# Performance work log

Hardware: AMD Instinct MI355X
Metric: run time of the kernel (lower is better)

The kernel has to match this reference:

```python
import jax, jax.numpy as jnp
import numpy as np

N_HEAD = 8
D_HEAD = 64
HIDDEN = 512
T = 2048
BS = 4
SCALE = D_HEAD ** -0.5


def setup_inputs() -> dict:
    key = jax.random.key(0)
    k1, k2, k3 = jax.random.split(key, 3)
    x = jax.random.normal(k1, (BS, T, HIDDEN), dtype=jnp.float32)
    # torch Linear weight is (out,in); we store as (in,out) for x @ W
    W_qkv = jax.random.normal(k2, (HIDDEN, (2 * N_HEAD + 1) * D_HEAD), dtype=jnp.float32) * 0.02
    W_out = jax.random.normal(k3, (D_HEAD, HIDDEN), dtype=jnp.float32) * 0.02
    return {"x": x, "W_qkv": W_qkv, "W_out": W_out}


def reference(x, W_qkv, W_out):
    bs, t, h = x.shape
    qkv = x @ W_qkv  # (bs, t, (2H+1)*d)
    q, k, v = jnp.split(qkv, [N_HEAD * D_HEAD, 2 * N_HEAD * D_HEAD], axis=-1)
    q = q.reshape(bs, t, N_HEAD, D_HEAD)
    k = k.reshape(bs, t, N_HEAD, D_HEAD)
    # v is shared across heads: (bs, t, d)
    score = jnp.einsum("bqhd,bkhd->bhqk", q, k) * SCALE
    causal = jnp.triu(jnp.full((t, t), -jnp.inf, dtype=score.dtype), 1)
    score = score + causal[None, None, :, :]
    prob = jax.nn.softmax(score, axis=-1)  # (bs, H, t, t)
    attn_vec = jnp.einsum("bhqk,bkd->bhqd", prob, v)  # shared V broadcast over heads
    m_attn_vec = jnp.mean(attn_vec, axis=1)  # head-mean: (bs, t, d)
    out = m_attn_vec @ W_out  # (bs, t, hidden)
    return out, attn_vec
```

## Files before the change

### kernel.cpp

```cpp
#include <hip/hip_runtime.h>
#include <hip/hip_bf16.h>

#define NHEAD  8
#define DHEAD  64
#define HIDDEN 512
#define SEQ_T  2048
#define BATCH  4
#define NQKV   1088
#define QPITCH 1152
#define NT     32
#define NROWS  (BATCH * SEQ_T)
#define NBH    (BATCH * NHEAD)
#define LPITCH (NBH * SEQ_T)
#define OSLICE ((size_t)NBH * SEQ_T * DHEAD)
#define QSC    (0.125f * 1.44269504f)

typedef __attribute__((ext_vector_type(8))) short short8;
typedef __attribute__((ext_vector_type(4))) float f32x4;

__device__ __forceinline__ unsigned short f2bf(float f) {
  unsigned int u = __float_as_uint(f);
  u += 0x7FFFu + ((u >> 16) & 1u);
  return (unsigned short)(u >> 16);
}
__device__ __forceinline__ float bf2f(unsigned short u) {
  return __uint_as_float((unsigned int)u << 16);
}

__device__ __forceinline__ void load_lds16(const unsigned short* g, unsigned short* l) {
  __builtin_amdgcn_global_load_lds((const __attribute__((address_space(1))) void*)g,
                                   (__attribute__((address_space(3))) void*)l, 16, 0, 0);
}

__global__ __launch_bounds__(256) void prep(const float* __restrict__ x,
                                            const float* __restrict__ W,
                                            const float* __restrict__ Wout,
                                            unsigned short* __restrict__ xb,
                                            unsigned short* __restrict__ Wt,
                                            unsigned short* __restrict__ Wob) {
  const int bx = blockIdx.x;
  const int tid = threadIdx.x;
  if (bx < 2048) {
    const size_t i0 = ((size_t)bx * 256 + tid) * 8;
    float4 a = *(const float4*)(x + i0);
    float4 b = *(const float4*)(x + i0 + 4);
    ushort4 u0, u1;
    u0.x = f2bf(a.x); u0.y = f2bf(a.y); u0.z = f2bf(a.z); u0.w = f2bf(a.w);
    u1.x = f2bf(b.x); u1.y = f2bf(b.y); u1.z = f2bf(b.z); u1.w = f2bf(b.w);
    *(ushort4*)(xb + i0) = u0;
    *(ushort4*)(xb + i0 + 4) = u1;
    return;
  }
  if (bx >= 2184 && bx < 2192) {
    const int z = bx - 2184;
    const size_t base = (size_t)NQKV * HIDDEN + ((size_t)z * 256 + tid) * 16;
    uint4 zero = {0u, 0u, 0u, 0u};
    *(uint4*)(Wt + base) = zero;
    *(uint4*)(Wt + base + 8) = zero;
    return;
  }
  if (bx >= 2192) {
    const int n0 = (bx - 2192) * 64;
    __shared__ float T[64 * 65];
#pragma unroll
    for (int i = 0; i < 4; ++i) {
      int f = tid + i * 256;
      int r = f >> 4;
      int c4 = (f & 15) * 4;
      float4 v = *(const float4*)(Wout + (size_t)r * HIDDEN + n0 + c4);
      T[r * 65 + c4 + 0] = v.x;
      T[r * 65 + c4 + 1] = v.y;
      T[r * 65 + c4 + 2] = v.z;
      T[r * 65 + c4 + 3] = v.w;
    }
    __syncthreads();
#pragma unroll
    for (int i = 0; i < 4; ++i) {
      int f = tid + i * 256;
      int n = f >> 4;
      int k4 = (f & 15) * 4;
      ushort4 u;
      u.x = f2bf(T[(k4 + 0) * 65 + n]);
      u.y = f2bf(T[(k4 + 1) * 65 + n]);
      u.z = f2bf(T[(k4 + 2) * 65 + n]);
      u.w = f2bf(T[(k4 + 3) * 65 + n]);
      *(ushort4*)(Wob + (size_t)(n0 + n) * DHEAD + k4) = u;
    }
    return;
  }
  const int idx = bx - 2048;
  const int n0 = (idx % 17) * 64;
  const int k0 = (idx / 17) * 64;
  __shared__ float T[64 * 65];
#pragma unroll
  for (int i = 0; i < 4; ++i) {
    int f = tid + i * 256;
    int r = f >> 4;
    int c4 = (f & 15) * 4;
    float4 v = *(const float4*)(W + (size_t)(k0 + r) * NQKV + n0 + c4);
    T[r * 65 + c4 + 0] = v.x;
    T[r * 65 + c4 + 1] = v.y;
    T[r * 65 + c4 + 2] = v.z;
    T[r * 65 + c4 + 3] = v.w;
  }
  __syncthreads();
#pragma unroll
  for (int i = 0; i < 4; ++i) {
    int f = tid + i * 256;
    int n = f >> 4;
    int k4 = (f & 15) * 4;
    ushort4 u;
    u.x = f2bf(T[(k4 + 0) * 65 + n]);
    u.y = f2bf(T[(k4 + 1) * 65 + n]);
    u.z = f2bf(T[(k4 + 2) * 65 + n]);
    u.w = f2bf(T[(k4 + 3) * 65 + n]);
    *(ushort4*)(Wt + (size_t)(n0 + n) * HIDDEN + k0 + k4) = u;
  }
}

__global__ __launch_bounds__(256, 3) void qkv_mfma(const unsigned short* __restrict__ Xb,
                                                   const unsigned short* __restrict__ Wt,
                                                   unsigned short* __restrict__ Y,
                                                   unsigned short* __restrict__ vt) {
  __shared__ __align__(16) unsigned short SH[2 * 128 * 64];
  unsigned short* As = SH;
  unsigned short* Bs = SH + 128 * 64;
  const int L = blockIdx.x;
  const int slot = L >> 3;
  const int bm = (L & 7) * 8 + (slot & 7);
  const int bn = slot >> 3;
  const int tid = threadIdx.x;
  const int wave = tid >> 6;
  const int lane = tid & 63;
  const int quad = lane >> 4;
  const int l15 = lane & 15;
  const int lrow = lane >> 3;
  const int lchunk = lane & 7;

  const unsigned short* xrow = Xb + (size_t)bm * 128 * HIDDEN;
  const unsigned short* wrow = Wt + (size_t)bn * 128 * HIDDEN;

  f32x4 acc[2][8];
#pragma unroll
  for (int mt = 0; mt < 2; ++mt)
#pragma unroll
    for (int nt = 0; nt < 8; ++nt) acc[mt][nt] = (f32x4){0.f, 0.f, 0.f, 0.f};

  for (int k0 = 0; k0 < HIDDEN; k0 += 64) {
    __syncthreads();
#pragma unroll
    for (int c = 0; c < 4; ++c) {
      int call = wave * 4 + c;
      int m = call * 8 + lrow;
      int clog = lchunk ^ lrow;
      load_lds16(xrow + (size_t)m * HIDDEN + k0 + clog * 8, &As[call * 512]);
      load_lds16(wrow + (size_t)m * HIDDEN + k0 + clog * 8, &Bs[call * 512]);
    }
    __syncthreads();

#pragma unroll
    for (int ks = 0; ks < 2; ++ks) {
      short8 a[2], b[8];
#pragma unroll
      for (int mt = 0; mt < 2; ++mt) {
        int m = wave * 32 + mt * 16 + l15;
        int phys = (ks * 4 + quad) ^ (l15 & 7);
        a[mt] = *(const short8*)&As[m * 64 + phys * 8];
      }
#pragma unroll
      for (int nt = 0; nt < 8; ++nt) {
        int n = nt * 16 + l15;
        int phys = (ks * 4 + quad) ^ (l15 & 7);
        b[nt] = *(const short8*)&Bs[n * 64 + phys * 8];
      }
#pragma unroll
      for (int mt = 0; mt < 2; ++mt)
#pragma unroll
        for (int nt = 0; nt < 8; ++nt)
          acc[mt][nt] = __builtin_amdgcn_mfma_f32_16x16x32_bf16(a[mt], b[nt], acc[mt][nt], 0, 0, 0);
    }
  }

  if (bn != 8) {
    const float qs = (bn < 4) ? QSC : 1.0f;
#pragma unroll
    for (int mt = 0; mt < 2; ++mt)
#pragma unroll
      for (int r = 0; r < 4; ++r) {
        int row = bm * 128 + wave * 32 + mt * 16 + quad * 4 + r;
#pragma unroll
        for (int nt = 0; nt < 8; ++nt) {
          int col = bn * 128 + nt * 16 + l15;
          Y[(size_t)row * QPITCH + col] = f2bf(acc[mt][nt][r] * qs);
        }
      }
  } else {
    __syncthreads();
    unsigned short* Vs = SH;
#pragma unroll
    for (int mt = 0; mt < 2; ++mt)
#pragma unroll
      for (int nt = 0; nt < 4; ++nt)
#pragma unroll
        for (int r = 0; r < 4; ++r) {
          int lr = wave * 32 + mt * 16 + quad * 4 + r;
          int d = nt * 16 + l15;
          Vs[d * 130 + lr] = f2bf(acc[mt][nt][r]);
        }
    __syncthreads();
    const int bb = bm >> 4;
    const int t0 = (bm & 15) * 128;
    const int half = lane >> 5;
    const int np = lane & 31;
    const int s2 = ((np & 16) << 1) | ((np & 2) << 3) | (np & 12) | ((np & 1) << 1);
#pragma unroll
    for (int i = 0; i < 16; ++i) {
      int d = i * 4 + wave;
      unsigned int v = *(const unsigned int*)&Vs[d * 130 + half * 64 + s2];
      *(unsigned int*)&vt[((size_t)bb * DHEAD + d) * SEQ_T + t0 + half * 64 + 2 * np] = v;
    }
  }
}

__global__ __launch_bounds__(256, 2) void attn_pass(const unsigned short* __restrict__ qkv,
                                                    const unsigned short* __restrict__ vt,
                                                    unsigned short* __restrict__ pbuf,
                                                    float* __restrict__ lbuf) {
  const int bh = blockIdx.x;
  const int yy = 19 - blockIdx.y;
  const int qt = (yy >= 1) + (yy >= 2) + (yy >= 4) + (yy >= 6) +
                 (yy >= 9) + (yy >= 12) + (yy >= 16);
  const int m = qt >> 1;
  const int Cq = (qt & 1) ? (m + 1) * (m + 1) : m * (m + 1);
  const int si = yy - Cq;
  const int ns = m + 1;
  const int ntile = 4 * qt + 4;
  const int kbeg = (si * ntile) / ns;
  const int kend = ((si + 1) * ntile) / ns - 1;

  const int b = bh >> 3;
  const int h = bh & 7;
  const int tid = threadIdx.x;
  const int wave = tid >> 6;
  const int lane = tid & 63;
  const int quad = lane >> 4;
  const int l15 = lane & 15;

  __shared__ __align__(16) unsigned short Ks[2][64 * 64];
  __shared__ __align__(16) unsigned short Vts[2][64 * 64];

  const unsigned short* bq = qkv + (size_t)b * SEQ_T * QPITCH;
  const unsigned short* bvt = vt + (size_t)b * DHEAD * SEQ_T;

  const int q0 = qt * 256;

  short8 aq[4][2];
#pragma unroll
  for (int s = 0; s < 4; ++s) {
    const unsigned short* qp = bq + (size_t)(q0 + s * 64 + wave * 16 + l15) * QPITCH + h * 64 + quad * 8;
    aq[s][0] = *(const short8*)qp;
    aq[s][1] = *(const short8*)(qp + 32);
  }

  f32x4 o[4][4];
#pragma unroll
  for (int s = 0; s < 4; ++s)
#pragma unroll
    for (int t = 0; t < 4; ++t) o[s][t] = (f32x4){0.f, 0.f, 0.f, 0.f};
  f32x4 ol[4];
#pragma unroll
  for (int s = 0; s < 4; ++s) ol[s] = (f32x4){0.f, 0.f, 0.f, 0.f};
  const short8 vone = {(short)0x3F80, (short)0x3F80, (short)0x3F80, (short)0x3F80,
                       (short)0x3F80, (short)0x3F80, (short)0x3F80, (short)0x3F80};

  const int srow = tid >> 3;
  const int sch = (tid & 7) ^ (srow & 7);
  const int ph0 = (quad ^ (l15 & 7)) * 8;

#pragma unroll
  for (int c = 0; c < 2; ++c) {
    load_lds16(bq + (size_t)(kbeg * 64 + c * 32 + srow) * QPITCH + 512 + h * 64 + sch * 8,
               &Ks[0][c * 2048 + wave * 512]);
    load_lds16(bvt + (size_t)(c * 32 + srow) * SEQ_T + kbeg * 64 + sch * 8,
               &Vts[0][c * 2048 + wave * 512]);
  }

  for (int kt = kbeg; kt <= kend; ++kt) {
    const int k0 = kt * 64;
    const int cur = (kt - kbeg) & 1;
    __syncthreads();
    if (kt < kend) {
      const int kn = (kt + 1) * 64;
      const int nxt = cur ^ 1;
#pragma unroll
      for (int c = 0; c < 2; ++c) {
        load_lds16(bq + (size_t)(kn + c * 32 + srow) * QPITCH + 512 + h * 64 + sch * 8,
                   &Ks[nxt][c * 2048 + wave * 512]);
        load_lds16(bvt + (size_t)(c * 32 + srow) * SEQ_T + kn + sch * 8,
                   &Vts[nxt][c * 2048 + wave * 512]);
      }
    }

    const unsigned short* ksb = Ks[cur];
    const unsigned short* vsb = Vts[cur];

    short8 bk[4][2], bv[4][2];
#pragma unroll
    for (int t = 0; t < 4; ++t) {
      const unsigned short* kp = &ksb[(l15 + 16 * t) * 64];
      bk[t][0] = *(const short8*)(kp + ph0);
      bk[t][1] = *(const short8*)(kp + (ph0 ^ 32));
      const unsigned short* vp = &vsb[(l15 + 16 * t) * 64];
      bv[t][0] = *(const short8*)(vp + ph0);
      bv[t][1] = *(const short8*)(vp + (ph0 ^ 32));
    }

#pragma unroll
    for (int s = 0; s < 4; ++s) {
      f32x4 pr[4];
#pragma unroll
      for (int t = 0; t < 4; ++t) {
        f32x4 sv = (f32x4){0.f, 0.f, 0.f, 0.f};
        sv = __builtin_amdgcn_mfma_f32_16x16x32_bf16(bk[t][0], aq[s][0], sv, 0, 0, 0);
        sv = __builtin_amdgcn_mfma_f32_16x16x32_bf16(bk[t][1], aq[s][1], sv, 0, 0, 0);
        pr[t] = sv;
      }
      const int qrow = q0 + s * 64 + wave * 16 + l15;
      const bool needMask = (k0 + 63) > (q0 + s * 64);
#pragma unroll
      for (int t = 0; t < 4; ++t)
#pragma unroll
        for (int r = 0; r < 4; ++r) {
          float p = __builtin_amdgcn_exp2f(pr[t][r]);
          if (needMask)
            p = (k0 + 16 * t + 4 * quad + r <= qrow) ? p : 0.f;
          pr[t][r] = p;
        }
      short8 ap[2];
#pragma unroll
      for (int c = 0; c < 2; ++c) {
        union { unsigned int u[4]; short8 v; } pk;
        pk.u[0] = __builtin_amdgcn_perm(__float_as_uint(pr[2 * c][1]),
                                        __float_as_uint(pr[2 * c][0]), 0x07060302u);
        pk.u[1] = __builtin_amdgcn_perm(__float_as_uint(pr[2 * c][3]),
                                        __float_as_uint(pr[2 * c][2]), 0x07060302u);
        pk.u[2] = __builtin_amdgcn_perm(__float_as_uint(pr[2 * c + 1][1]),
                                        __float_as_uint(pr[2 * c + 1][0]), 0x07060302u);
        pk.u[3] = __builtin_amdgcn_perm(__float_as_uint(pr[2 * c + 1][3]),
                                        __float_as_uint(pr[2 * c + 1][2]), 0x07060302u);
        ap[c] = pk.v;
      }
      ol[s] = __builtin_amdgcn_mfma_f32_16x16x32_bf16(ap[0], vone, ol[s], 0, 0, 0);
      ol[s] = __builtin_amdgcn_mfma_f32_16x16x32_bf16(ap[1], vone, ol[s], 0, 0, 0);
#pragma unroll
      for (int t = 0; t < 4; ++t) {
        o[s][t] = __builtin_amdgcn_mfma_f32_16x16x32_bf16(ap[0], bv[t][0], o[s][t], 0, 0, 0);
        o[s][t] = __builtin_amdgcn_mfma_f32_16x16x32_bf16(ap[1], bv[t][1], o[s][t], 0, 0, 0);
      }
    }
  }

  unsigned short* pb = pbuf + (size_t)si * OSLICE;
#pragma unroll
  for (int s = 0; s < 4; ++s) {
#pragma unroll
    for (int r = 0; r < 4; ++r) {
      const int trow = q0 + s * 64 + wave * 16 + quad * 4 + r;
      if (l15 == 0) lbuf[si * LPITCH + bh * SEQ_T + trow] = ol[s][r];
      const size_t base = ((size_t)bh * SEQ_T + trow) * DHEAD;
#pragma unroll
      for (int t = 0; t < 4; ++t) pb[base + l15 + 16 * t] = f2bf(o[s][t][r]);
    }
  }
}

__global__ __launch_bounds__(256) void out_merge(const unsigned short* __restrict__ pbuf,
                                                 const float* __restrict__ lbuf,
                                                 const unsigned short* __restrict__ Wob,
                                                 float* __restrict__ attnv,
                                                 float* __restrict__ out) {
  const int row0 = blockIdx.x * 16;
  const int tid = threadIdx.x;
  __shared__ float Ms[16][66];

  {
    const int lr = tid >> 4;
    const int d0 = (tid & 15) * 4;
    const int row = row0 + lr;
    const int b = row >> 11;
    const int t = row & 2047;
    const int ns = (t >> 9) + 1;
    float s0 = 0.f, s1 = 0.f, s2 = 0.f, s3 = 0.f;
#pragma unroll
    for (int hh = 0; hh < NHEAD; ++hh) {
      const size_t ridx = (size_t)(b * NHEAD + hh) * SEQ_T + t;
      float l = 0.f;
      float4 macc = {0.f, 0.f, 0.f, 0.f};
      const size_t idx = ridx * DHEAD + d0;
#pragma unroll
      for (int si = 0; si < 4; ++si) {
        if (si < ns) {
          l += lbuf[si * LPITCH + ridx];
          ushort4 A = *(const ushort4*)(pbuf + si * OSLICE + idx);
          macc.x += bf2f(A.x);
          macc.y += bf2f(A.y);
          macc.z += bf2f(A.z);
          macc.w += bf2f(A.w);
        }
      }
      const float inv = 1.0f / l;
      float4 mv;
      mv.x = macc.x * inv;
      mv.y = macc.y * inv;
      mv.z = macc.z * inv;
      mv.w = macc.w * inv;
      *(float4*)(attnv + idx) = mv;
      s0 += mv.x; s1 += mv.y; s2 += mv.z; s3 += mv.w;
    }
    Ms[lr][d0 + 0] = s0 * 0.125f;
    Ms[lr][d0 + 1] = s1 * 0.125f;
    Ms[lr][d0 + 2] = s2 * 0.125f;
    Ms[lr][d0 + 3] = s3 * 0.125f;
  }
  __syncthreads();

  const int wv = tid >> 6;
  const int lane = tid & 63;
  const int quad = lane >> 4;
  const int l15 = lane & 15;

  short8 am[2];
  {
    union { unsigned short us[16]; short8 v[2]; } u;
#pragma unroll
    for (int j = 0; j < 8; ++j) {
      u.us[j] = f2bf(Ms[l15][quad * 8 + j]);
      u.us[8 + j] = f2bf(Ms[l15][32 + quad * 8 + j]);
    }
    am[0] = u.v[0];
    am[1] = u.v[1];
  }

#pragma unroll
  for (int nt = 0; nt < 8; ++nt) {
    const int n = wv * 128 + nt * 16 + l15;
    short8 b0 = *(const short8*)&Wob[(size_t)n * DHEAD + quad * 8];
    short8 b1 = *(const short8*)&Wob[(size_t)n * DHEAD + 32 + quad * 8];
    f32x4 c = (f32x4){0.f, 0.f, 0.f, 0.f};
    c = __builtin_amdgcn_mfma_f32_16x16x32_bf16(am[0], b0, c, 0, 0, 0);
    c = __builtin_amdgcn_mfma_f32_16x16x32_bf16(am[1], b1, c, 0, 0, 0);
#pragma unroll
    for (int r = 0; r < 4; ++r)
      out[(size_t)(row0 + quad * 4 + r) * HIDDEN + n] = c[r];
  }
}

extern "C" void kernel_launch(void* const* d_in, const int* in_sizes, int n_in,
                              void* d_out, int out_size, void* d_ws, size_t ws_size,
                              hipStream_t stream) {
  const float* x     = (const float*)d_in[0];
  const float* W_qkv = (const float*)d_in[1];
  const float* W_out = (const float*)d_in[2];

  float* out      = (float*)d_out;
  float* attn_vec = out + (size_t)BATCH * SEQ_T * HIDDEN;

  unsigned short* qkv  = (unsigned short*)d_ws;
  unsigned short* vt   = qkv + (size_t)NROWS * QPITCH;
  unsigned short* xb   = vt + (size_t)BATCH * DHEAD * SEQ_T;
  unsigned short* Wt   = xb + (size_t)NROWS * HIDDEN;
  unsigned short* pbuf = Wt + (size_t)QPITCH * HIDDEN;
  float*          lbuf = (float*)(pbuf + 4 * OSLICE);
  unsigned short* Wob  = (unsigned short*)(lbuf + 4 * LPITCH);

  prep<<<dim3(2048 + 136 + 8 + 8), 256, 0, stream>>>(x, W_qkv, W_out, xb, Wt, Wob);
  qkv_mfma<<<dim3(576), 256, 0, stream>>>(xb, Wt, qkv, vt);
  attn_pass<<<dim3(NBH, 20), 256, 0, stream>>>(qkv, vt, pbuf, lbuf);
  out_merge<<<dim3(512), 256, 0, stream>>>(pbuf, lbuf, Wob, attn_vec, out);
}
```

Before: 148.2 us.

## Shrink attention query tiles to 128 rows and rebalance KV split scheduling

The attention pass now handles 128 query rows per block instead of 256. Its KV-split map changes to 1, 2 or 3 splits per query tile, for 32 y-blocks per head, and the merge kernel and buffers are updated to match. The occupancy hint rises to 3 blocks per CU, and the V fragment loads move after the softmax so fewer registers are live at once. The V-column block of the QKV GEMM also stops loading and multiplying the unused half of the weight tile. The trade-off is more blocks and more K/V reloads per query row in exchange for better load balance and occupancy.

```diff
diff --git a/kernel.cpp b/kernel.cpp
--- a/kernel.cpp
+++ b/kernel.cpp
@@ -140,48 +140,48 @@
   const unsigned short* xrow = Xb + (size_t)bm * 128 * HIDDEN;
   const unsigned short* wrow = Wt + (size_t)bn * 128 * HIDDEN;
 
-  f32x4 acc[2][8];
-#pragma unroll
-  for (int mt = 0; mt < 2; ++mt)
-#pragma unroll
-    for (int nt = 0; nt < 8; ++nt) acc[mt][nt] = (f32x4){0.f, 0.f, 0.f, 0.f};
-
-  for (int k0 = 0; k0 < HIDDEN; k0 += 64) {
-    __syncthreads();
-#pragma unroll
-    for (int c = 0; c < 4; ++c) {
-      int call = wave * 4 + c;
-      int m = call * 8 + lrow;
-      int clog = lchunk ^ lrow;
-      load_lds16(xrow + (size_t)m * HIDDEN + k0 + clog * 8, &As[call * 512]);
-      load_lds16(wrow + (size_t)m * HIDDEN + k0 + clog * 8, &Bs[call * 512]);
-    }
-    __syncthreads();
-
-#pragma unroll
-    for (int ks = 0; ks < 2; ++ks) {
-      short8 a[2], b[8];
-#pragma unroll
-      for (int mt = 0; mt < 2; ++mt) {
-        int m = wave * 32 + mt * 16 + l15;
-        int phys = (ks * 4 + quad) ^ (l15 & 7);
-        a[mt] = *(const short8*)&As[m * 64 + phys * 8];
-      }
-#pragma unroll
-      for (int nt = 0; nt < 8; ++nt) {
-        int n = nt * 16 + l15;
-        int phys = (ks * 4 + quad) ^ (l15 & 7);
-        b[nt] = *(const short8*)&Bs[n * 64 + phys * 8];
-      }
-#pragma unroll
-      for (int mt = 0; mt < 2; ++mt)
-#pragma unroll
-        for (int nt = 0; nt < 8; ++nt)
-          acc[mt][nt] = __builtin_amdgcn_mfma_f32_16x16x32_bf16(a[mt], b[nt], acc[mt][nt], 0, 0, 0);
-    }
-  }
-
   if (bn != 8) {
+    f32x4 acc[2][8];
+#pragma unroll
+    for (int mt = 0; mt < 2; ++mt)
+#pragma unroll
+      for (int nt = 0; nt < 8; ++nt) acc[mt][nt] = (f32x4){0.f, 0.f, 0.f, 0.f};
+
+    for (int k0 = 0; k0 < HIDDEN; k0 += 64) {
+      __syncthreads();
+#pragma unroll
+      for (int c = 0; c < 4; ++c) {
+        int call = wave * 4 + c;
+        int m = call * 8 + lrow;
+        int clog = lchunk ^ lrow;
+        load_lds16(xrow + (size_t)m * HIDDEN + k0 + clog * 8, &As[call * 512]);
+        load_lds16(wrow + (size_t)m * HIDDEN + k0 + clog * 8, &Bs[call * 512]);
+      }
+      __syncthreads();
+
+#pragma unroll
+      for (int ks = 0; ks < 2; ++ks) {
+        short8 a[2], b[8];
+#pragma unroll
+        for (int mt = 0; mt < 2; ++mt) {
+          int m = wave * 32 + mt * 16 + l15;
+          int phys = (ks * 4 + quad) ^ (l15 & 7);
+          a[mt] = *(const short8*)&As[m * 64 + phys * 8];
+        }
+#pragma unroll
+        for (int nt = 0; nt < 8; ++nt) {
+          int n = nt * 16 + l15;
+          int phys = (ks * 4 + quad) ^ (l15 & 7);
+          b[nt] = *(const short8*)&Bs[n * 64 + phys * 8];
+        }
+#pragma unroll
+        for (int mt = 0; mt < 2; ++mt)
+#pragma unroll
+          for (int nt = 0; nt < 8; ++nt)
+            acc[mt][nt] = __builtin_amdgcn_mfma_f32_16x16x32_bf16(a[mt], b[nt], acc[mt][nt], 0, 0, 0);
+      }
+    }
+
     const float qs = (bn < 4) ? QSC : 1.0f;
 #pragma unroll
     for (int mt = 0; mt < 2; ++mt)
@@ -195,6 +195,48 @@
         }
       }
   } else {
+    f32x4 acc[2][4];
+#pragma unroll
+    for (int mt = 0; mt < 2; ++mt)
+#pragma unroll
+      for (int nt = 0; nt < 4; ++nt) acc[mt][nt] = (f32x4){0.f, 0.f, 0.f, 0.f};
+
+    for (int k0 = 0; k0 < HIDDEN; k0 += 64) {
+      __syncthreads();
+#pragma unroll
+      for (int c = 0; c < 4; ++c) {
+        int call = wave * 4 + c;
+        int m = call * 8 + lrow;
+        int clog = lchunk ^ lrow;
+        load_lds16(xrow + (size_t)m * HIDDEN + k0 + clog * 8, &As[call * 512]);
+        if (wave < 2)
+          load_lds16(wrow + (size_t)m * HIDDEN + k0 + clog * 8, &Bs[call * 512]);
+      }
+      __syncthreads();
+
+#pragma unroll
+      for (int ks = 0; ks < 2; ++ks) {
+        short8 a[2], b[4];
+#pragma unroll
+        for (int mt = 0; mt < 2; ++mt) {
+          int m = wave * 32 + mt * 16 + l15;
+          int phys = (ks * 4 + quad) ^ (l15 & 7);
+          a[mt] = *(const short8*)&As[m * 64 + phys * 8];
+        }
+#pragma unroll
+        for (int nt = 0; nt < 4; ++nt) {
+          int n = nt * 16 + l15;
+          int phys = (ks * 4 + quad) ^ (l15 & 7);
+          b[nt] = *(const short8*)&Bs[n * 64 + phys * 8];
+        }
+#pragma unroll
+        for (int mt = 0; mt < 2; ++mt)
+#pragma unroll
+          for (int nt = 0; nt < 4; ++nt)
+            acc[mt][nt] = __builtin_amdgcn_mfma_f32_16x16x32_bf16(a[mt], b[nt], acc[mt][nt], 0, 0, 0);
+      }
+    }
+
     __syncthreads();
     unsigned short* Vs = SH;
 #pragma unroll
@@ -222,19 +264,17 @@
   }
 }
 
-__global__ __launch_bounds__(256, 2) void attn_pass(const unsigned short* __restrict__ qkv,
+__global__ __launch_bounds__(256, 3) void attn_pass(const unsigned short* __restrict__ qkv,
                                                     const unsigned short* __restrict__ vt,
                                                     unsigned short* __restrict__ pbuf,
                                                     float* __restrict__ lbuf) {
   const int bh = blockIdx.x;
-  const int yy = 19 - blockIdx.y;
-  const int qt = (yy >= 1) + (yy >= 2) + (yy >= 4) + (yy >= 6) +
-                 (yy >= 9) + (yy >= 12) + (yy >= 16);
-  const int m = qt >> 1;
-  const int Cq = (qt & 1) ? (m + 1) * (m + 1) : m * (m + 1);
-  const int si = yy - Cq;
-  const int ns = m + 1;
-  const int ntile = 4 * qt + 4;
+  const int yy = 31 - blockIdx.y;
+  int qt, si, ns;
+  if (yy < 4)       { qt = yy;                 si = 0;            ns = 1; }
+  else if (yy < 20) { qt = 4 + ((yy - 4) >> 1); si = (yy - 4) & 1; ns = 2; }
+  else              { qt = 12 + (yy - 20) / 3;  si = (yy - 20) % 3; ns = 3; }
+  const int ntile = 2 * qt + 2;
   const int kbeg = (si * ntile) / ns;
   const int kend = ((si + 1) * ntile) / ns - 1;
 
@@ -252,24 +292,22 @@
   const unsigned short* bq = qkv + (size_t)b * SEQ_T * QPITCH;
   const unsigned short* bvt = vt + (size_t)b * DHEAD * SEQ_T;
 
-  const int q0 = qt * 256;
-
-  short8 aq[4][2];
-#pragma unroll
-  for (int s = 0; s < 4; ++s) {
+  const int q0 = qt * 128;
+
+  short8 aq[2][2];
+#pragma unroll
+  for (int s = 0; s < 2; ++s) {
     const unsigned short* qp = bq + (size_t)(q0 + s * 64 + wave * 16 + l15) * QPITCH + h * 64 + quad * 8;
     aq[s][0] = *(const short8*)qp;
     aq[s][1] = *(const short8*)(qp + 32);
   }
 
-  f32x4 o[4][4];
-#pragma unroll
-  for (int s = 0; s < 4; ++s)
+  f32x4 o[2][4];
+#pragma unroll
+  for (int s = 0; s < 2; ++s)
 #pragma unroll
     for (int t = 0; t < 4; ++t) o[s][t] = (f32x4){0.f, 0.f, 0.f, 0.f};
-  f32x4 ol[4];
-#pragma unroll
-  for (int s = 0; s < 4; ++s) ol[s] = (f32x4){0.f, 0.f, 0.f, 0.f};
+  f32x4 ol[2] = {(f32x4){0.f, 0.f, 0.f, 0.f}, (f32x4){0.f, 0.f, 0.f, 0.f}};
   const short8 vone = {(short)0x3F80, (short)0x3F80, (short)0x3F80, (short)0x3F80,
                        (short)0x3F80, (short)0x3F80, (short)0x3F80, (short)0x3F80};
 
@@ -303,20 +341,19 @@
 
     const unsigned short* ksb = Ks[cur];
     const unsigned short* vsb = Vts[cur];
-
-    short8 bk[4][2], bv[4][2];
+    const bool needMask = (k0 + 63) > q0;
+
+    short8 bk[4][2];
 #pragma unroll
     for (int t = 0; t < 4; ++t) {
       const unsigned short* kp = &ksb[(l15 + 16 * t) * 64];
       bk[t][0] = *(const short8*)(kp + ph0);
       bk[t][1] = *(const short8*)(kp + (ph0 ^ 32));
-      const unsigned short* vp = &vsb[(l15 + 16 * t) * 64];
-      bv[t][0] = *(const short8*)(vp + ph0);
-      bv[t][1] = *(const short8*)(vp + (ph0 ^ 32));
-    }
-
-#pragma unroll
-    for (int s = 0; s < 4; ++s) {
+    }
+
+    short8 ap[2][2];
+#pragma unroll
+    for (int s = 0; s < 2; ++s) {
       f32x4 pr[4];
 #pragma unroll
       for (int t = 0; t < 4; ++t) {
@@ -326,7 +363,6 @@
         pr[t] = sv;
       }
       const int qrow = q0 + s * 64 + wave * 16 + l15;
-      const bool needMask = (k0 + 63) > (q0 + s * 64);
 #pragma unroll
       for (int t = 0; t < 4; ++t)
 #pragma unroll
@@ -336,7 +372,6 @@
             p = (k0 + 16 * t + 4 * quad + r <= qrow) ? p : 0.f;
           pr[t][r] = p;
         }
-      short8 ap[2];
 #pragma unroll
       for (int c = 0; c < 2; ++c) {
         union { unsigned int u[4]; short8 v; } pk;
@@ -348,21 +383,32 @@
                                         __float_as_uint(pr[2 * c + 1][0]), 0x07060302u);
         pk.u[3] = __builtin_amdgcn_perm(__float_as_uint(pr[2 * c + 1][3]),
                                         __float_as_uint(pr[2 * c + 1][2]), 0x07060302u);
-        ap[c] = pk.v;
-      }
-      ol[s] = __builtin_amdgcn_mfma_f32_16x16x32_bf16(ap[0], vone, ol[s], 0, 0, 0);
-      ol[s] = __builtin_amdgcn_mfma_f32_16x16x32_bf16(ap[1], vone, ol[s], 0, 0, 0);
-#pragma unroll
-      for (int t = 0; t < 4; ++t) {
-        o[s][t] = __builtin_amdgcn_mfma_f32_16x16x32_bf16(ap[0], bv[t][0], o[s][t], 0, 0, 0);
-        o[s][t] = __builtin_amdgcn_mfma_f32_16x16x32_bf16(ap[1], bv[t][1], o[s][t], 0, 0, 0);
-      }
-    }
+        ap[s][c] = pk.v;
+      }
+      ol[s] = __builtin_amdgcn_mfma_f32_16x16x32_bf16(ap[s][0], vone, ol[s], 0, 0, 0);
+      ol[s] = __builtin_amdgcn_mfma_f32_16x16x32_bf16(ap[s][1], vone, ol[s], 0, 0, 0);
+    }
+
+    short8 bv[4][2];
+#pragma unroll
+    for (int t = 0; t < 4; ++t) {
+      const unsigned short* vp = &vsb[(l15 + 16 * t) * 64];
+      bv[t][0] = *(const short8*)(vp + ph0);
+      bv[t][1] = *(const short8*)(vp + (ph0 ^ 32));
+    }
+
+#pragma unroll
+    for (int t = 0; t < 4; ++t)
+#pragma unroll
+      for (int s = 0; s < 2; ++s) {
+        o[s][t] = __builtin_amdgcn_mfma_f32_16x16x32_bf16(ap[s][0], bv[t][0], o[s][t], 0, 0, 0);
+        o[s][t] = __builtin_amdgcn_mfma_f32_16x16x32_bf16(ap[s][1], bv[t][1], o[s][t], 0, 0, 0);
+      }
   }
 
   unsigned short* pb = pbuf + (size_t)si * OSLICE;
 #pragma unroll
-  for (int s = 0; s < 4; ++s) {
+  for (int s = 0; s < 2; ++s) {
 #pragma unroll
     for (int r = 0; r < 4; ++r) {
       const int trow = q0 + s * 64 + wave * 16 + quad * 4 + r;
@@ -389,7 +435,8 @@
     const int row = row0 + lr;
     const int b = row >> 11;
     const int t = row & 2047;
-    const int ns = (t >> 9) + 1;
+    const int qt = t >> 7;
+    const int ns = 1 + (qt >= 4 ? 1 : 0) + (qt >= 12 ? 1 : 0);
     float s0 = 0.f, s1 = 0.f, s2 = 0.f, s3 = 0.f;
 #pragma unroll
     for (int hh = 0; hh < NHEAD; ++hh) {
@@ -398,7 +445,7 @@
       float4 macc = {0.f, 0.f, 0.f, 0.f};
       const size_t idx = ridx * DHEAD + d0;
 #pragma unroll
-      for (int si = 0; si < 4; ++si) {
+      for (int si = 0; si < 3; ++si) {
         if (si < ns) {
           l += lbuf[si * LPITCH + ridx];
           ushort4 A = *(const ushort4*)(pbuf + si * OSLICE + idx);
@@ -470,11 +517,11 @@
   unsigned short* xb   = vt + (size_t)BATCH * DHEAD * SEQ_T;
   unsigned short* Wt   = xb + (size_t)NROWS * HIDDEN;
   unsigned short* pbuf = Wt + (size_t)QPITCH * HIDDEN;
-  float*          lbuf = (float*)(pbuf + 4 * OSLICE);
-  unsigned short* Wob  = (unsigned short*)(lbuf + 4 * LPITCH);
+  float*          lbuf = (float*)(pbuf + 3 * OSLICE);
+  unsigned short* Wob  = (unsigned short*)(lbuf + 3 * LPITCH);
 
   prep<<<dim3(2048 + 136 + 8 + 8), 256, 0, stream>>>(x, W_qkv, W_out, xb, Wt, Wob);
   qkv_mfma<<<dim3(576), 256, 0, stream>>>(xb, Wt, qkv, vt);
-  attn_pass<<<dim3(NBH, 20), 256, 0, stream>>>(qkv, vt, pbuf, lbuf);
+  attn_pass<<<dim3(NBH, 32), 256, 0, stream>>>(qkv, vt, pbuf, lbuf);
   out_merge<<<dim3(512), 256, 0, stream>>>(pbuf, lbuf, Wob, attn_vec, out);
 }
```

Result: faster. 135.4 us (-8.6%).
